# Kernel optimization log

Hardware: AMD Instinct MI355X
Metric: run time of the kernel (lower is better)

The kernel has to match this reference:

```python
import jax, jax.numpy as jnp
import numpy as np

D = 768
H = 16
DH = D // H  # 48
SCALE = 1.0 / np.sqrt(DH).astype(np.float32)
EPS = 1e-3  # keras LayerNormalization default epsilon
NEG = -1e9


def setup_inputs() -> dict:
    key = jax.random.key(0)
    ks = jax.random.split(key, 10)
    B, S = 4, 2048
    q = jax.random.normal(ks[0], (B, S, D), dtype=jnp.float32)
    k = jax.random.normal(ks[1], (B, S, D), dtype=jnp.float32)
    v = jax.random.normal(ks[2], (B, S, D), dtype=jnp.float32)
    # Dense projection params (glorot-ish scale)
    w_std = 1.0 / np.sqrt(D)
    Wq = jax.random.normal(ks[3], (D, D), dtype=jnp.float32) * w_std
    Wk = jax.random.normal(ks[4], (D, D), dtype=jnp.float32) * w_std
    Wv = jax.random.normal(ks[5], (D, D), dtype=jnp.float32) * w_std
    bq = jnp.zeros((D,), jnp.float32)
    bk = jnp.zeros((D,), jnp.float32)
    bv = jnp.zeros((D,), jnp.float32)
    gamma = jnp.ones((D,), jnp.float32)
    beta = jnp.zeros((D,), jnp.float32)
    return {"q": q, "k": k, "v": v, "Wq": Wq, "bq": bq, "Wk": Wk, "bk": bk,
            "Wv": Wv, "bv": bv, "gamma": gamma, "beta": beta}


def reference(q, k, v, Wq, bq, Wk, bk, Wv, bv, gamma, beta):
    use_causal = True  # exercise the causal-mask path
    B, S, _ = q.shape
    # Projections, then split into heads (tf.split on last axis == reshape)
    Q = (q @ Wq + bq).reshape(B, S, H, DH)
    K = (k @ Wk + bk).reshape(B, S, H, DH)
    V = (v @ Wv + bv).reshape(B, S, H, DH)
    # scores: [B, H, Sq, Sk]
    scores = jnp.einsum('bqhd,bkhd->bhqk', Q, K) * SCALE
    if use_causal:
        qi = jnp.arange(S)[:, None]
        ki = jnp.arange(S)[None, :]
        mask = jnp.where(qi >= ki, 0.0, NEG).astype(scores.dtype)
        scores = scores + mask
    attn = jax.nn.softmax(scores, axis=-1)
    out = jnp.einsum('bhqk,bkhd->bqhd', attn, V).reshape(B, S, D)
    # LayerNorm over last dim
    mu = jnp.mean(out, axis=-1, keepdims=True)
    var = jnp.mean(jnp.square(out - mu), axis=-1, keepdims=True)
    return (out - mu) * jax.lax.rsqrt(var + EPS) * gamma + beta
```

## Files before the change

### kernel.cpp

```cpp
#include <hip/hip_runtime.h>
#include <hip/hip_bf16.h>


#define DMODEL 768
#define NHEAD  16
#define DHEAD  48
#define SEQ    2048
#define NBATCH 4
#define NROWS  (NBATCH * SEQ)
#define QSCALE (0.14433756729740643f * 1.4426950408889634f)

typedef __bf16 bf16x8 __attribute__((ext_vector_type(8)));
typedef float  f32x4  __attribute__((ext_vector_type(4)));

__global__ __launch_bounds__(256) void transpose_w(
    const float* __restrict__ Wq,
    const float* __restrict__ Wk,
    const float* __restrict__ Wv,
    __hip_bfloat16* __restrict__ Wt)
{
    __shared__ __hip_bfloat16 tile[32][33];
    int bid = blockIdx.x;
    int mat = bid / 576;
    int t   = bid - mat * 576;
    int tr  = t / 24, tc = t - (t / 24) * 24;
    const float* W = (mat == 0) ? Wq : (mat == 1) ? Wk : Wv;
    __hip_bfloat16* O = Wt + (size_t)mat * DMODEL * DMODEL;
    int tx = threadIdx.x & 31, ty = threadIdx.x >> 5;
#pragma unroll
    for (int i = 0; i < 32; i += 8)
        tile[ty + i][tx] = __float2bfloat16(W[(size_t)(tr * 32 + ty + i) * DMODEL + tc * 32 + tx]);
    __syncthreads();
#pragma unroll
    for (int i = 0; i < 32; i += 8)
        O[(size_t)(tc * 32 + ty + i) * DMODEL + tr * 32 + tx] = tile[tx][ty + i];
}

__global__ __launch_bounds__(256, 2) void qkv_proj(
    const float* __restrict__ xq,
    const float* __restrict__ xk,
    const float* __restrict__ xv,
    const __hip_bfloat16* __restrict__ Wt,
    const float* __restrict__ bq,
    const float* __restrict__ bk,
    const float* __restrict__ bv,
    __hip_bfloat16* __restrict__ Qr,
    __hip_bfloat16* __restrict__ Kr,
    __hip_bfloat16* __restrict__ Vt)
{
    __shared__ __hip_bfloat16 As[2][128 * 32];
    __shared__ __hip_bfloat16 Bs[2][128 * 32];

    int xcd  = blockIdx.x & 7;
    int s    = blockIdx.x >> 3;
    int nt   = s % 6;
    int pair = (s / 6) * 8 + xcd;
    int mat  = pair >> 6;
    int mt   = pair & 63;
    int m0   = mt * 128, n0 = nt * 128;

    const float* X          = (mat == 0) ? xq : (mat == 1) ? xk : xv;
    const __hip_bfloat16* W = Wt + (size_t)mat * DMODEL * DMODEL;
    const float* bias       = (mat == 0) ? bq : (mat == 1) ? bk : bv;

    int tid  = threadIdx.x;
    int w    = tid >> 6, lane = tid & 63;
    int l16  = lane & 15, quad = lane >> 4;
    int wm   = w >> 1, wn = w & 1;

    int rS = tid >> 1;
    int cS = (tid & 1) << 4;
    const float*          xb = X + (size_t)(m0 + rS) * DMODEL + cS;
    const __hip_bfloat16* wb = W + (size_t)(n0 + rS) * DMODEL + cS;
    int ldsOff = rS * 32 + cS;

    float4 fA0, fA1, fA2, fA3;
    uint4  rB0, rB1;

#define QKV_LOAD(k0_) {                                                        \
        fA0 = *(const float4*)(xb + (k0_));                                    \
        fA1 = *(const float4*)(xb + (k0_) + 4);                                \
        fA2 = *(const float4*)(xb + (k0_) + 8);                                \
        fA3 = *(const float4*)(xb + (k0_) + 12);                               \
        rB0 = *(const uint4*)(wb + (k0_));                                     \
        rB1 = *(const uint4*)(wb + (k0_) + 8); }

#define QKV_STORE(buf_) {                                                      \
        *(bf16x8*)&As[buf_][ldsOff] =                                          \
            (bf16x8){ (__bf16)fA0.x, (__bf16)fA0.y, (__bf16)fA0.z, (__bf16)fA0.w, \
                      (__bf16)fA1.x, (__bf16)fA1.y, (__bf16)fA1.z, (__bf16)fA1.w }; \
        *(bf16x8*)&As[buf_][ldsOff + 8] =                                      \
            (bf16x8){ (__bf16)fA2.x, (__bf16)fA2.y, (__bf16)fA2.z, (__bf16)fA2.w, \
                      (__bf16)fA3.x, (__bf16)fA3.y, (__bf16)fA3.z, (__bf16)fA3.w }; \
        *(uint4*)&Bs[buf_][ldsOff]     = rB0;                                  \
        *(uint4*)&Bs[buf_][ldsOff + 8] = rB1; }

    f32x4 acc[4][4] = {};

    QKV_LOAD(0);
    QKV_STORE(0);
    QKV_LOAD(32);
    __syncthreads();

    for (int it = 0; it < 24; ++it) {
        int buf = it & 1;
        if (it + 1 < 24) QKV_STORE(buf ^ 1);
        if (it + 2 < 24) QKV_LOAD((it + 2) * 32);

        bf16x8 a[4], b[4];
#pragma unroll
        for (int i = 0; i < 4; ++i)
            a[i] = *(const bf16x8*)&As[buf][(wm * 64 + i * 16 + l16) * 32 + quad * 8];
#pragma unroll
        for (int j = 0; j < 4; ++j)
            b[j] = *(const bf16x8*)&Bs[buf][(wn * 64 + j * 16 + l16) * 32 + quad * 8];
#pragma unroll
        for (int i = 0; i < 4; ++i)
#pragma unroll
            for (int j = 0; j < 4; ++j)
                acc[i][j] = __builtin_amdgcn_mfma_f32_16x16x32_bf16(a[i], b[j], acc[i][j], 0, 0, 0);

        __syncthreads();
    }
#undef QKV_LOAD
#undef QKV_STORE

#pragma unroll
    for (int j = 0; j < 4; ++j) {
        int col = n0 + wn * 64 + j * 16 + l16;
        float bc = bias[col];
        if (mat == 0) {
#pragma unroll
            for (int i = 0; i < 4; ++i) {
                int row0 = m0 + wm * 64 + i * 16 + quad * 4;
#pragma unroll
                for (int r = 0; r < 4; ++r)
                    Qr[(size_t)(row0 + r) * DMODEL + col] =
                        __float2bfloat16((acc[i][j][r] + bc) * QSCALE);
            }
        } else if (mat == 1) {
#pragma unroll
            for (int i = 0; i < 4; ++i) {
                int row0 = m0 + wm * 64 + i * 16 + quad * 4;
#pragma unroll
                for (int r = 0; r < 4; ++r)
                    Kr[(size_t)(row0 + r) * DMODEL + col] =
                        __float2bfloat16(acc[i][j][r] + bc);
            }
        } else {
            int h = col / 48, dh = col - h * 48;
#pragma unroll
            for (int i = 0; i < 4; ++i) {
                int row0 = m0 + wm * 64 + i * 16 + quad * 4;
                int bb = row0 >> 11, s0 = row0 & 2047;
                ushort4 pk;
                union { __hip_bfloat16 b; unsigned short u; } cv;
                cv.b = __float2bfloat16(acc[i][j][0] + bc); pk.x = cv.u;
                cv.b = __float2bfloat16(acc[i][j][1] + bc); pk.y = cv.u;
                cv.b = __float2bfloat16(acc[i][j][2] + bc); pk.z = cv.u;
                cv.b = __float2bfloat16(acc[i][j][3] + bc); pk.w = cv.u;
                *(ushort4*)(Vt + ((size_t)(bb * NHEAD + h) * DHEAD + dh) * SEQ + s0) = pk;
            }
        }
    }
}

__global__ __launch_bounds__(256, 3) void attn(
    const __hip_bfloat16* __restrict__ Qr,
    const __hip_bfloat16* __restrict__ Kr,
    const __hip_bfloat16* __restrict__ Vt,
    __hip_bfloat16* __restrict__ Ao)
{
    __shared__ __hip_bfloat16 Ks[2][64][72];
    __shared__ __hip_bfloat16 Vs[2][48][72];
    __shared__ __hip_bfloat16 Ps[4][32][72];

    int tid  = threadIdx.x;
    int w    = tid >> 6, lane = tid & 63;
    int l16  = lane & 15, quad = lane >> 4;
    int bh   = blockIdx.x & 63;
    int qt   = 15 - (blockIdx.x >> 6);
    int q0   = qt * 128;
    int b    = bh >> 4, h = bh & 15;
    size_t rowbase = (size_t)b * SEQ;

    const __hip_bfloat16* Qp = Qr + rowbase * DMODEL + h * DHEAD;
    const __hip_bfloat16* Kp = Kr + rowbase * DMODEL + h * DHEAD;
    const __hip_bfloat16* Vp = Vt + (size_t)bh * DHEAD * SEQ;

    for (int idx = tid; idx < 1024; idx += 256) {
        int buf = idx >> 9, r = (idx >> 3) & 63, c = idx & 7;
        ((unsigned int*)&Ks[buf][r][48])[c] = 0u;
    }

    bf16x8 bQ0[2], bQ1[2];
#pragma unroll
    for (int i = 0; i < 2; ++i) {
        int qrow = q0 + w * 32 + i * 16 + l16;
        bQ0[i] = *(const bf16x8*)(Qp + (size_t)qrow * DMODEL + quad * 8);
        bQ1[i] = (bf16x8){};
        if (quad < 2)
            bQ1[i] = *(const bf16x8*)(Qp + (size_t)qrow * DMODEL + 32 + quad * 8);
    }

    int rK = tid >> 2, oK = (tid & 3) * 12;
    int dV = tid >> 3, oV = (tid & 7) * 8;

    uint2 kr0, kr1, kr2; uint4 vr0, vr1;

#define ATTN_LOAD(kt_) {                                                        \
        int k0_ = (kt_) * 64;                                                   \
        const __hip_bfloat16* kb_ = Kp + (size_t)(k0_ + rK) * DMODEL + oK;      \
        kr0 = *(const uint2*)(kb_);                                             \
        kr1 = *(const uint2*)(kb_ + 4);                                         \
        kr2 = *(const uint2*)(kb_ + 8);                                         \
        vr0 = *(const uint4*)(Vp + (size_t)dV * SEQ + k0_ + oV);                \
        if (tid < 128) vr1 = *(const uint4*)(Vp + (size_t)(32 + dV) * SEQ + k0_ + oV); }

#define ATTN_STORE(buf_) {                                                      \
        __hip_bfloat16* kd_ = &Ks[buf_][rK][oK];                                \
        *(uint2*)(kd_)     = kr0;                                               \
        *(uint2*)(kd_ + 4) = kr1;                                               \
        *(uint2*)(kd_ + 8) = kr2;                                               \
        *(uint4*)&Vs[buf_][dV][oV] = vr0;                                       \
        if (tid < 128) *(uint4*)&Vs[buf_][32 + dV][oV] = vr1; }

    f32x4 O[2][3] = {};
    float lsum[2] = {0.f, 0.f};

    int ktmax = 2 * qt + 1;
    ATTN_LOAD(0);
    ATTN_STORE(0);
    if (ktmax >= 1) ATTN_LOAD(1);
    __syncthreads();

    for (int kt = 0; kt <= ktmax; ++kt) {
        int buf = kt & 1;
        int k0  = kt * 64;
        if (kt + 1 <= ktmax) ATTN_STORE(buf ^ 1);
        if (kt + 2 <= ktmax) ATTN_LOAD(kt + 2);

        bf16x8 aK0[4], aK1[4];
#pragma unroll
        for (int t = 0; t < 4; ++t) {
            aK0[t] = *(const bf16x8*)&Ks[buf][16 * t + l16][quad * 8];
            aK1[t] = *(const bf16x8*)&Ks[buf][16 * t + l16][32 + quad * 8];
        }

#pragma unroll
        for (int i = 0; i < 2; ++i) {
            int qbase = q0 + w * 32 + i * 16;
            if (k0 > qbase + 15) continue;

            f32x4 s[4];
#pragma unroll
            for (int t = 0; t < 4; ++t) {
                f32x4 z = {};
                z    = __builtin_amdgcn_mfma_f32_16x16x32_bf16(aK0[t], bQ0[i], z, 0, 0, 0);
                s[t] = __builtin_amdgcn_mfma_f32_16x16x32_bf16(aK1[t], bQ1[i], z, 0, 0, 0);
            }

            if (k0 + 63 > qbase) {
                int qg = qbase + l16;
#pragma unroll
                for (int t = 0; t < 4; ++t) {
                    int kg = k0 + 16 * t + quad * 4;
#pragma unroll
                    for (int r = 0; r < 4; ++r)
                        if (kg + r > qg) s[t][r] = -1e30f;
                }
            }

            float ls = 0.f;
#pragma unroll
            for (int t = 0; t < 4; ++t) {
                float p0 = exp2f(s[t][0]), p1 = exp2f(s[t][1]);
                float p2 = exp2f(s[t][2]), p3 = exp2f(s[t][3]);
                ls += (p0 + p1) + (p2 + p3);
                union { __bf16 hv[4]; uint2 u2; } pk;
                pk.hv[0] = (__bf16)p0; pk.hv[1] = (__bf16)p1;
                pk.hv[2] = (__bf16)p2; pk.hv[3] = (__bf16)p3;
                *(uint2*)&Ps[w][i * 16 + l16][16 * t + quad * 4] = pk.u2;
            }
            lsum[i] += ls;
        }

        bf16x8 bV0[3], bV1[3];
#pragma unroll
        for (int dt = 0; dt < 3; ++dt) {
            bV0[dt] = *(const bf16x8*)&Vs[buf][dt * 16 + l16][quad * 8];
            bV1[dt] = *(const bf16x8*)&Vs[buf][dt * 16 + l16][32 + quad * 8];
        }

#pragma unroll
        for (int i = 0; i < 2; ++i) {
            int qbase = q0 + w * 32 + i * 16;
            if (k0 > qbase + 15) continue;
            bf16x8 aP0 = *(const bf16x8*)&Ps[w][i * 16 + l16][quad * 8];
            bf16x8 aP1 = *(const bf16x8*)&Ps[w][i * 16 + l16][32 + quad * 8];
#pragma unroll
            for (int dt = 0; dt < 3; ++dt) {
                O[i][dt] = __builtin_amdgcn_mfma_f32_16x16x32_bf16(aP0, bV0[dt], O[i][dt], 0, 0, 0);
                O[i][dt] = __builtin_amdgcn_mfma_f32_16x16x32_bf16(aP1, bV1[dt], O[i][dt], 0, 0, 0);
            }
        }

        __syncthreads();
    }

#pragma unroll
    for (int i = 0; i < 2; ++i) {
        lsum[i] += __shfl_xor(lsum[i], 16, 64);
        lsum[i] += __shfl_xor(lsum[i], 32, 64);
    }

#pragma unroll
    for (int i = 0; i < 2; ++i) {
#pragma unroll
        for (int r = 0; r < 4; ++r) {
            float linv = 1.f / __shfl(lsum[i], quad * 4 + r, 64);
            size_t g = (rowbase + q0 + w * 32 + i * 16 + quad * 4 + r) * DMODEL + h * DHEAD + l16;
            Ao[g + 0]  = __float2bfloat16(O[i][0][r] * linv);
            Ao[g + 16] = __float2bfloat16(O[i][1][r] * linv);
            Ao[g + 32] = __float2bfloat16(O[i][2][r] * linv);
        }
    }
#undef ATTN_LOAD
#undef ATTN_STORE
}

__global__ __launch_bounds__(192) void lnorm(
    const __hip_bfloat16* __restrict__ Ao,
    const float* __restrict__ gamma,
    const float* __restrict__ beta,
    float* __restrict__ out)
{
    __shared__ float rs_[3], rq_[3];
    int row = blockIdx.x;
    int t   = threadIdx.x;
    size_t base = (size_t)row * DMODEL + t * 4;

    ushort4 u = *(const ushort4*)(Ao + base);
    float x0, x1, x2, x3;
    { unsigned int v = (unsigned int)u.x << 16; __builtin_memcpy(&x0, &v, 4); }
    { unsigned int v = (unsigned int)u.y << 16; __builtin_memcpy(&x1, &v, 4); }
    { unsigned int v = (unsigned int)u.z << 16; __builtin_memcpy(&x2, &v, 4); }
    { unsigned int v = (unsigned int)u.w << 16; __builtin_memcpy(&x3, &v, 4); }

    float s = x0 + x1 + x2 + x3;
    float q = x0 * x0 + x1 * x1 + x2 * x2 + x3 * x3;
#pragma unroll
    for (int m = 32; m >= 1; m >>= 1) {
        s += __shfl_xor(s, m, 64);
        q += __shfl_xor(q, m, 64);
    }
    int wv = t >> 6;
    if ((t & 63) == 0) { rs_[wv] = s; rq_[wv] = q; }
    __syncthreads();
    float ts = rs_[0] + rs_[1] + rs_[2];
    float tq = rq_[0] + rq_[1] + rq_[2];
    float mu  = ts * (1.f / 768.f);
    float var = tq * (1.f / 768.f) - mu * mu;
    float rstd = rsqrtf(var + 1e-3f);

    float4 g  = *(const float4*)(gamma + t * 4);
    float4 be = *(const float4*)(beta + t * 4);
    float4 o;
    o.x = (x0 - mu) * rstd * g.x + be.x;
    o.y = (x1 - mu) * rstd * g.y + be.y;
    o.z = (x2 - mu) * rstd * g.z + be.z;
    o.w = (x3 - mu) * rstd * g.w + be.w;
    *(float4*)(out + base) = o;
}

extern "C" void kernel_launch(void* const* d_in, const int* in_sizes, int n_in,
                              void* d_out, int out_size, void* d_ws, size_t ws_size,
                              hipStream_t stream) {
    const float* q     = (const float*)d_in[0];
    const float* k     = (const float*)d_in[1];
    const float* v     = (const float*)d_in[2];
    const float* Wq    = (const float*)d_in[3];
    const float* bq    = (const float*)d_in[4];
    const float* Wk    = (const float*)d_in[5];
    const float* bk    = (const float*)d_in[6];
    const float* Wv    = (const float*)d_in[7];
    const float* bv    = (const float*)d_in[8];
    const float* gamma = (const float*)d_in[9];
    const float* beta  = (const float*)d_in[10];

    char* basep = (char*)d_ws;
    __hip_bfloat16* Wt = (__hip_bfloat16*)basep;
    __hip_bfloat16* Qr = (__hip_bfloat16*)(basep + 3538944);
    __hip_bfloat16* Kr = Qr + (size_t)NROWS * DMODEL;
    __hip_bfloat16* Vt = Kr + (size_t)NROWS * DMODEL;
    __hip_bfloat16* Ao = Vt + (size_t)NROWS * DMODEL;
    float* out = (float*)d_out;

    hipLaunchKernelGGL(transpose_w, dim3(1728), dim3(256), 0, stream, Wq, Wk, Wv, Wt);
    hipLaunchKernelGGL(qkv_proj, dim3(1152), dim3(256), 0, stream,
                       q, k, v, Wt, bq, bk, bv, Qr, Kr, Vt);
    hipLaunchKernelGGL(attn, dim3(1024), dim3(256), 0, stream, Qr, Kr, Vt, Ao);
    hipLaunchKernelGGL(lnorm, dim3(8192), dim3(192), 0, stream, Ao, gamma, beta, out);
}
```

Measured before the change: 265.6 us.

## Swizzle QKV GEMM LDS layout, double-register prefetch, and use lighter barriers

The QKV projection GEMM now stages tiles with an XOR-swizzled LDS layout, so the MFMA fragment reads avoid bank conflicts. The loop is unrolled by two with two register sets (A/B), so global loads for tile k+2 are in flight while tile k is computed. __syncthreads is replaced by an explicit lgkmcnt wait plus s_barrier, here and in the attention loop, so outstanding global loads (vmcnt) are not drained at each barrier. This raises register pressure and depends on the manual wait being enough for correctness.

```diff
diff --git a/kernel.cpp b/kernel.cpp
--- a/kernel.cpp
+++ b/kernel.cpp
@@ -67,63 +67,82 @@
     int w    = tid >> 6, lane = tid & 63;
     int l16  = lane & 15, quad = lane >> 4;
     int wm   = w >> 1, wn = w & 1;
-
-    int rS = tid >> 1;
-    int cS = (tid & 1) << 4;
-    const float*          xb = X + (size_t)(m0 + rS) * DMODEL + cS;
-    const __hip_bfloat16* wb = W + (size_t)(n0 + rS) * DMODEL + cS;
-    int ldsOff = rS * 32 + cS;
-
-    float4 fA0, fA1, fA2, fA3;
-    uint4  rB0, rB1;
-
-#define QKV_LOAD(k0_) {                                                        \
-        fA0 = *(const float4*)(xb + (k0_));                                    \
-        fA1 = *(const float4*)(xb + (k0_) + 4);                                \
-        fA2 = *(const float4*)(xb + (k0_) + 8);                                \
-        fA3 = *(const float4*)(xb + (k0_) + 12);                               \
-        rB0 = *(const uint4*)(wb + (k0_));                                     \
-        rB1 = *(const uint4*)(wb + (k0_) + 8); }
-
-#define QKV_STORE(buf_) {                                                      \
-        *(bf16x8*)&As[buf_][ldsOff] =                                          \
-            (bf16x8){ (__bf16)fA0.x, (__bf16)fA0.y, (__bf16)fA0.z, (__bf16)fA0.w, \
-                      (__bf16)fA1.x, (__bf16)fA1.y, (__bf16)fA1.z, (__bf16)fA1.w }; \
-        *(bf16x8*)&As[buf_][ldsOff + 8] =                                      \
-            (bf16x8){ (__bf16)fA2.x, (__bf16)fA2.y, (__bf16)fA2.z, (__bf16)fA2.w, \
-                      (__bf16)fA3.x, (__bf16)fA3.y, (__bf16)fA3.z, (__bf16)fA3.w }; \
-        *(uint4*)&Bs[buf_][ldsOff]     = rB0;                                  \
-        *(uint4*)&Bs[buf_][ldsOff + 8] = rB1; }
+    int qs   = quad ^ ((l16 >> 1) & 3);
+
+    int w0 = tid, w1 = tid + 256;
+    int r0 = w0 >> 2, k0c = (w0 & 3) ^ ((w0 >> 3) & 3);
+    int r1 = w1 >> 2, k1c = (w1 & 3) ^ ((w1 >> 3) & 3);
+    const float*          xb0 = X + (size_t)(m0 + r0) * DMODEL + k0c * 8;
+    const float*          xb1 = X + (size_t)(m0 + r1) * DMODEL + k1c * 8;
+    const __hip_bfloat16* wb0 = W + (size_t)(n0 + r0) * DMODEL + k0c * 8;
+    const __hip_bfloat16* wb1 = W + (size_t)(n0 + r1) * DMODEL + k1c * 8;
+
+    float4 fA0A, fA1A, fA2A, fA3A; uint4 rB0A, rB1A;
+    float4 fA0B, fA1B, fA2B, fA3B; uint4 rB0B, rB1B;
+
+#define QKV_LOAD(kt_, S) {                                                     \
+        fA0##S = *(const float4*)(xb0 + (kt_) * 32);                           \
+        fA1##S = *(const float4*)(xb0 + (kt_) * 32 + 4);                       \
+        fA2##S = *(const float4*)(xb1 + (kt_) * 32);                           \
+        fA3##S = *(const float4*)(xb1 + (kt_) * 32 + 4);                       \
+        rB0##S = *(const uint4*)(wb0 + (kt_) * 32);                            \
+        rB1##S = *(const uint4*)(wb1 + (kt_) * 32); }
+
+#define QKV_STORE(buf_, S) {                                                   \
+        *(bf16x8*)&As[buf_][w0 * 8] =                                          \
+            (bf16x8){ (__bf16)fA0##S.x, (__bf16)fA0##S.y, (__bf16)fA0##S.z, (__bf16)fA0##S.w, \
+                      (__bf16)fA1##S.x, (__bf16)fA1##S.y, (__bf16)fA1##S.z, (__bf16)fA1##S.w }; \
+        *(bf16x8*)&As[buf_][w1 * 8] =                                          \
+            (bf16x8){ (__bf16)fA2##S.x, (__bf16)fA2##S.y, (__bf16)fA2##S.z, (__bf16)fA2##S.w, \
+                      (__bf16)fA3##S.x, (__bf16)fA3##S.y, (__bf16)fA3##S.z, (__bf16)fA3##S.w }; \
+        *(uint4*)&Bs[buf_][w0 * 8] = rB0##S;                                   \
+        *(uint4*)&Bs[buf_][w1 * 8] = rB1##S; }
+
+#define QKV_MATH(buf_) {                                                       \
+        bf16x8 a[4], b[4];                                                     \
+        _Pragma("unroll")                                                      \
+        for (int i = 0; i < 4; ++i)                                            \
+            a[i] = *(const bf16x8*)&As[buf_][(wm * 64 + i * 16 + l16) * 32 + qs * 8]; \
+        _Pragma("unroll")                                                      \
+        for (int j = 0; j < 4; ++j)                                            \
+            b[j] = *(const bf16x8*)&Bs[buf_][(wn * 64 + j * 16 + l16) * 32 + qs * 8]; \
+        _Pragma("unroll")                                                      \
+        for (int i = 0; i < 4; ++i)                                            \
+        _Pragma("unroll")                                                      \
+        for (int j = 0; j < 4; ++j)                                            \
+            acc[i][j] = __builtin_amdgcn_mfma_f32_16x16x32_bf16(a[i], b[j], acc[i][j], 0, 0, 0); }
+
+#define QKV_BARRIER() {                                                        \
+        asm volatile("s_waitcnt lgkmcnt(0)" ::: "memory");                     \
+        __builtin_amdgcn_s_barrier();                                          \
+        asm volatile("" ::: "memory"); }
 
     f32x4 acc[4][4] = {};
 
-    QKV_LOAD(0);
-    QKV_STORE(0);
-    QKV_LOAD(32);
-    __syncthreads();
-
-    for (int it = 0; it < 24; ++it) {
-        int buf = it & 1;
-        if (it + 1 < 24) QKV_STORE(buf ^ 1);
-        if (it + 2 < 24) QKV_LOAD((it + 2) * 32);
-
-        bf16x8 a[4], b[4];
-#pragma unroll
-        for (int i = 0; i < 4; ++i)
-            a[i] = *(const bf16x8*)&As[buf][(wm * 64 + i * 16 + l16) * 32 + quad * 8];
-#pragma unroll
-        for (int j = 0; j < 4; ++j)
-            b[j] = *(const bf16x8*)&Bs[buf][(wn * 64 + j * 16 + l16) * 32 + quad * 8];
-#pragma unroll
-        for (int i = 0; i < 4; ++i)
-#pragma unroll
-            for (int j = 0; j < 4; ++j)
-                acc[i][j] = __builtin_amdgcn_mfma_f32_16x16x32_bf16(a[i], b[j], acc[i][j], 0, 0, 0);
-
-        __syncthreads();
-    }
+    QKV_LOAD(0, A);
+    QKV_STORE(0, A);
+    QKV_LOAD(1, B);
+    QKV_BARRIER();
+
+    for (int it = 0; it < 22; it += 2) {
+        QKV_LOAD(it + 2, A);
+        QKV_STORE(1, B);
+        QKV_MATH(0);
+        QKV_BARRIER();
+        QKV_LOAD(it + 3, B);
+        QKV_STORE(0, A);
+        QKV_MATH(1);
+        QKV_BARRIER();
+    }
+    QKV_STORE(1, B);
+    QKV_MATH(0);
+    QKV_BARRIER();
+    QKV_MATH(1);
+
 #undef QKV_LOAD
 #undef QKV_STORE
+#undef QKV_MATH
+#undef QKV_BARRIER
 
 #pragma unroll
     for (int j = 0; j < 4; ++j) {
@@ -305,7 +324,9 @@
             }
         }
 
-        __syncthreads();
+        asm volatile("s_waitcnt lgkmcnt(0)" ::: "memory");
+        __builtin_amdgcn_s_barrier();
+        asm volatile("" ::: "memory");
     }
 
 #pragma unroll
```

After: 264.4 us. About the same (-0.5%).

## Pre-convert inputs to bf16 and pipeline QKV GEMM with direct global-to-LDS loads

Applied to the files above, without the earlier changes.

A prep kernel now converts the activations to bf16 in scratch space (reusing the output and attention buffers) alongside the weight transpose. The QKV projection is restructured into 512-thread 256x128 tiles that use global_load_lds with a triple-buffered A and double-buffered B, split MFMA phases with priority boosts and explicit waitcnt/barriers. This removes the fp32 register staging and in-loop conversion, and moves more of the loads off the register path. In exchange it adds an extra bf16 write and read of the activations. The attention loop barrier is also replaced with an explicit lgkmcnt wait plus s_barrier.

```diff
diff --git a/kernel.cpp b/kernel.cpp
--- a/kernel.cpp
+++ b/kernel.cpp
@@ -13,33 +13,56 @@
 typedef __bf16 bf16x8 __attribute__((ext_vector_type(8)));
 typedef float  f32x4  __attribute__((ext_vector_type(4)));
 
-__global__ __launch_bounds__(256) void transpose_w(
+__global__ __launch_bounds__(256) void prep(
     const float* __restrict__ Wq,
     const float* __restrict__ Wk,
     const float* __restrict__ Wv,
-    __hip_bfloat16* __restrict__ Wt)
-{
-    __shared__ __hip_bfloat16 tile[32][33];
-    int bid = blockIdx.x;
-    int mat = bid / 576;
-    int t   = bid - mat * 576;
-    int tr  = t / 24, tc = t - (t / 24) * 24;
-    const float* W = (mat == 0) ? Wq : (mat == 1) ? Wk : Wv;
-    __hip_bfloat16* O = Wt + (size_t)mat * DMODEL * DMODEL;
-    int tx = threadIdx.x & 31, ty = threadIdx.x >> 5;
-#pragma unroll
-    for (int i = 0; i < 32; i += 8)
-        tile[ty + i][tx] = __float2bfloat16(W[(size_t)(tr * 32 + ty + i) * DMODEL + tc * 32 + tx]);
-    __syncthreads();
-#pragma unroll
-    for (int i = 0; i < 32; i += 8)
-        O[(size_t)(tc * 32 + ty + i) * DMODEL + tr * 32 + tx] = tile[tx][ty + i];
-}
-
-__global__ __launch_bounds__(256, 2) void qkv_proj(
     const float* __restrict__ xq,
     const float* __restrict__ xk,
     const float* __restrict__ xv,
+    __hip_bfloat16* __restrict__ Wt,
+    __hip_bfloat16* __restrict__ Xbq,
+    __hip_bfloat16* __restrict__ Xbk,
+    __hip_bfloat16* __restrict__ Xbv)
+{
+    int bid = blockIdx.x;
+    if (bid < 1728) {
+        __shared__ __hip_bfloat16 tile[32][33];
+        int mat = bid / 576;
+        int t   = bid - mat * 576;
+        int tr  = t / 24, tc = t - (t / 24) * 24;
+        const float* W = (mat == 0) ? Wq : (mat == 1) ? Wk : Wv;
+        __hip_bfloat16* O = Wt + (size_t)mat * DMODEL * DMODEL;
+        int tx = threadIdx.x & 31, ty = threadIdx.x >> 5;
+#pragma unroll
+        for (int i = 0; i < 32; i += 8)
+            tile[ty + i][tx] = __float2bfloat16(W[(size_t)(tr * 32 + ty + i) * DMODEL + tc * 32 + tx]);
+        __syncthreads();
+#pragma unroll
+        for (int i = 0; i < 32; i += 8)
+            O[(size_t)(tc * 32 + ty + i) * DMODEL + tr * 32 + tx] = tile[tx][ty + i];
+    } else {
+        int b2  = bid - 1728;
+        int mat = b2 / 3072;
+        int r   = b2 - mat * 3072;
+        const float* X = (mat == 0) ? xq : (mat == 1) ? xk : xv;
+        __hip_bfloat16* O = (mat == 0) ? Xbq : (mat == 1) ? Xbk : Xbv;
+        size_t off = (size_t)r * 2048 + threadIdx.x * 8;
+        float4 f0 = *(const float4*)(X + off);
+        float4 f1 = *(const float4*)(X + off + 4);
+        union { __hip_bfloat16 h[8]; uint4 u; } pk;
+        pk.h[0] = __float2bfloat16(f0.x); pk.h[1] = __float2bfloat16(f0.y);
+        pk.h[2] = __float2bfloat16(f0.z); pk.h[3] = __float2bfloat16(f0.w);
+        pk.h[4] = __float2bfloat16(f1.x); pk.h[5] = __float2bfloat16(f1.y);
+        pk.h[6] = __float2bfloat16(f1.z); pk.h[7] = __float2bfloat16(f1.w);
+        *(uint4*)(O + off) = pk.u;
+    }
+}
+
+__global__ __launch_bounds__(512, 4) void qkv_proj(
+    const __hip_bfloat16* __restrict__ Xbq,
+    const __hip_bfloat16* __restrict__ Xbk,
+    const __hip_bfloat16* __restrict__ Xbv,
     const __hip_bfloat16* __restrict__ Wt,
     const float* __restrict__ bq,
     const float* __restrict__ bk,
@@ -48,82 +71,100 @@
     __hip_bfloat16* __restrict__ Kr,
     __hip_bfloat16* __restrict__ Vt)
 {
-    __shared__ __hip_bfloat16 As[2][128 * 32];
-    __shared__ __hip_bfloat16 Bs[2][128 * 32];
-
-    int xcd  = blockIdx.x & 7;
-    int s    = blockIdx.x >> 3;
-    int nt   = s % 6;
-    int pair = (s / 6) * 8 + xcd;
-    int mat  = pair >> 6;
-    int mt   = pair & 63;
-    int m0   = mt * 128, n0 = nt * 128;
-
-    const float* X          = (mat == 0) ? xq : (mat == 1) ? xk : xv;
-    const __hip_bfloat16* W = Wt + (size_t)mat * DMODEL * DMODEL;
-    const float* bias       = (mat == 0) ? bq : (mat == 1) ? bk : bv;
+    __shared__ __hip_bfloat16 Abuf[3][8192];
+    __shared__ __hip_bfloat16 Bbuf[2][4096];
 
     int tid  = threadIdx.x;
     int w    = tid >> 6, lane = tid & 63;
     int l16  = lane & 15, quad = lane >> 4;
     int wm   = w >> 1, wn = w & 1;
 
-    int rS = tid >> 1;
-    int cS = (tid & 1) << 4;
-    const float*          xb = X + (size_t)(m0 + rS) * DMODEL + cS;
-    const __hip_bfloat16* wb = W + (size_t)(n0 + rS) * DMODEL + cS;
-    int ldsOff = rS * 32 + cS;
-
-    float4 fA0, fA1, fA2, fA3;
-    uint4  rB0, rB1;
-
-#define QKV_LOAD(k0_) {                                                        \
-        fA0 = *(const float4*)(xb + (k0_));                                    \
-        fA1 = *(const float4*)(xb + (k0_) + 4);                                \
-        fA2 = *(const float4*)(xb + (k0_) + 8);                                \
-        fA3 = *(const float4*)(xb + (k0_) + 12);                               \
-        rB0 = *(const uint4*)(wb + (k0_));                                     \
-        rB1 = *(const uint4*)(wb + (k0_) + 8); }
-
-#define QKV_STORE(buf_) {                                                      \
-        *(bf16x8*)&As[buf_][ldsOff] =                                          \
-            (bf16x8){ (__bf16)fA0.x, (__bf16)fA0.y, (__bf16)fA0.z, (__bf16)fA0.w, \
-                      (__bf16)fA1.x, (__bf16)fA1.y, (__bf16)fA1.z, (__bf16)fA1.w }; \
-        *(bf16x8*)&As[buf_][ldsOff + 8] =                                      \
-            (bf16x8){ (__bf16)fA2.x, (__bf16)fA2.y, (__bf16)fA2.z, (__bf16)fA2.w, \
-                      (__bf16)fA3.x, (__bf16)fA3.y, (__bf16)fA3.z, (__bf16)fA3.w }; \
-        *(uint4*)&Bs[buf_][ldsOff]     = rB0;                                  \
-        *(uint4*)&Bs[buf_][ldsOff + 8] = rB1; }
+    int xcd = blockIdx.x & 7, s = blockIdx.x >> 3;
+    int nt  = s % 6;
+    int idx = (s / 6) * 8 + xcd;
+    int mat = idx >> 5, mt = idx & 31;
+    int m0  = mt * 256, n0 = nt * 128;
+
+    const __hip_bfloat16* X = (mat == 0) ? Xbq : (mat == 1) ? Xbk : Xbv;
+    const __hip_bfloat16* W = Wt + (size_t)mat * DMODEL * DMODEL;
+    const float* bias       = (mat == 0) ? bq : (mat == 1) ? bk : bv;
+
+    int sr = tid >> 2, sc = (tid & 3) * 8;
+    const __hip_bfloat16* ga0 = X + (size_t)(m0 + sr) * DMODEL + sc;
+    const __hip_bfloat16* ga1 = X + (size_t)(m0 + 128 + sr) * DMODEL + sc;
+    const __hip_bfloat16* gb  = W + (size_t)(n0 + sr) * DMODEL + sc;
+
+#define GLD(gp_, lp_) __builtin_amdgcn_global_load_lds(                        \
+        (const __attribute__((address_space(1))) void*)(gp_),                  \
+        (__attribute__((address_space(3))) void*)(lp_), 16, 0, 0)
+
+    int aoff = (wm * 64 + l16) * 32 + quad * 8;
+    int boff = (wn * 64 + l16) * 32 + quad * 8;
 
     f32x4 acc[4][4] = {};
 
-    QKV_LOAD(0);
-    QKV_STORE(0);
-    QKV_LOAD(32);
-    __syncthreads();
-
-    for (int it = 0; it < 24; ++it) {
-        int buf = it & 1;
-        if (it + 1 < 24) QKV_STORE(buf ^ 1);
-        if (it + 2 < 24) QKV_LOAD((it + 2) * 32);
-
-        bf16x8 a[4], b[4];
-#pragma unroll
-        for (int i = 0; i < 4; ++i)
-            a[i] = *(const bf16x8*)&As[buf][(wm * 64 + i * 16 + l16) * 32 + quad * 8];
-#pragma unroll
-        for (int j = 0; j < 4; ++j)
-            b[j] = *(const bf16x8*)&Bs[buf][(wn * 64 + j * 16 + l16) * 32 + quad * 8];
-#pragma unroll
-        for (int i = 0; i < 4; ++i)
-#pragma unroll
-            for (int j = 0; j < 4; ++j)
-                acc[i][j] = __builtin_amdgcn_mfma_f32_16x16x32_bf16(a[i], b[j], acc[i][j], 0, 0, 0);
-
-        __syncthreads();
-    }
-#undef QKV_LOAD
-#undef QKV_STORE
+    GLD(gb,       &Bbuf[0][tid * 8]);
+    GLD(ga0,      &Abuf[0][tid * 8]);
+    GLD(ga1,      &Abuf[0][4096 + tid * 8]);
+    GLD(ga0 + 32, &Abuf[1][tid * 8]);
+    GLD(ga1 + 32, &Abuf[1][4096 + tid * 8]);
+    asm volatile("s_waitcnt vmcnt(2)" ::: "memory");
+    asm volatile("s_barrier" ::: "memory");
+
+    int abuf = 0, bbuf = 0, abS = 2;
+    const __hip_bfloat16* gbS  = gb  + 32;
+    const __hip_bfloat16* ga0S = ga0 + 64;
+    const __hip_bfloat16* ga1S = ga1 + 64;
+
+    for (int kt = 0; kt < 24; ++kt) {
+        const __hip_bfloat16* LA = Abuf[abuf];
+        const __hip_bfloat16* LB = Bbuf[bbuf];
+
+        bf16x8 a[4], bA[2];
+#pragma unroll
+        for (int m_ = 0; m_ < 4; ++m_)
+            a[m_] = *(const bf16x8*)&LA[aoff + m_ * 512];
+        bA[0] = *(const bf16x8*)&LB[boff];
+        bA[1] = *(const bf16x8*)&LB[boff + 512];
+
+        if (kt < 23) { GLD(gbS, &Bbuf[bbuf ^ 1][tid * 8]); gbS += 32; }
+        if (kt < 22) {
+            GLD(ga0S, &Abuf[abS][tid * 8]);
+            GLD(ga1S, &Abuf[abS][4096 + tid * 8]);
+            ga0S += 32; ga1S += 32;
+        }
+
+        asm volatile("s_barrier" ::: "memory");
+        __builtin_amdgcn_s_setprio(1);
+#pragma unroll
+        for (int m_ = 0; m_ < 4; ++m_) {
+            acc[m_][0] = __builtin_amdgcn_mfma_f32_16x16x32_bf16(a[m_], bA[0], acc[m_][0], 0, 0, 0);
+            acc[m_][1] = __builtin_amdgcn_mfma_f32_16x16x32_bf16(a[m_], bA[1], acc[m_][1], 0, 0, 0);
+        }
+        __builtin_amdgcn_s_setprio(0);
+        asm volatile("s_barrier" ::: "memory");
+
+        bf16x8 bB[2];
+        bB[0] = *(const bf16x8*)&LB[boff + 1024];
+        bB[1] = *(const bf16x8*)&LB[boff + 1536];
+
+        if (kt < 22) asm volatile("s_waitcnt vmcnt(2)" ::: "memory");
+        else         asm volatile("s_waitcnt vmcnt(0)" ::: "memory");
+        asm volatile("s_barrier" ::: "memory");
+        __builtin_amdgcn_s_setprio(1);
+#pragma unroll
+        for (int m_ = 0; m_ < 4; ++m_) {
+            acc[m_][2] = __builtin_amdgcn_mfma_f32_16x16x32_bf16(a[m_], bB[0], acc[m_][2], 0, 0, 0);
+            acc[m_][3] = __builtin_amdgcn_mfma_f32_16x16x32_bf16(a[m_], bB[1], acc[m_][3], 0, 0, 0);
+        }
+        __builtin_amdgcn_s_setprio(0);
+        asm volatile("s_barrier" ::: "memory");
+
+        abuf = (abuf == 2) ? 0 : abuf + 1;
+        abS  = (abS  == 2) ? 0 : abS  + 1;
+        bbuf ^= 1;
+    }
+#undef GLD
 
 #pragma unroll
     for (int j = 0; j < 4; ++j) {
@@ -305,7 +346,9 @@
             }
         }
 
-        __syncthreads();
+        asm volatile("s_waitcnt lgkmcnt(0)" ::: "memory");
+        __builtin_amdgcn_s_barrier();
+        asm volatile("" ::: "memory");
     }
 
 #pragma unroll
@@ -396,9 +439,14 @@
     __hip_bfloat16* Ao = Vt + (size_t)NROWS * DMODEL;
     float* out = (float*)d_out;
 
-    hipLaunchKernelGGL(transpose_w, dim3(1728), dim3(256), 0, stream, Wq, Wk, Wv, Wt);
-    hipLaunchKernelGGL(qkv_proj, dim3(1152), dim3(256), 0, stream,
-                       q, k, v, Wt, bq, bk, bv, Qr, Kr, Vt);
+    __hip_bfloat16* Xbq = (__hip_bfloat16*)d_out;
+    __hip_bfloat16* Xbk = Xbq + (size_t)NROWS * DMODEL;
+    __hip_bfloat16* Xbv = Ao;
+
+    hipLaunchKernelGGL(prep, dim3(10944), dim3(256), 0, stream,
+                       Wq, Wk, Wv, q, k, v, Wt, Xbq, Xbk, Xbv);
+    hipLaunchKernelGGL(qkv_proj, dim3(576), dim3(512), 0, stream,
+                       Xbq, Xbk, Xbv, Wt, bq, bk, bv, Qr, Kr, Vt);
     hipLaunchKernelGGL(attn, dim3(1024), dim3(256), 0, stream, Qr, Kr, Vt, Ao);
     hipLaunchKernelGGL(lnorm, dim3(8192), dim3(192), 0, stream, Ao, gamma, beta, out);
 }
```

Result: faster. 256.3 us (-3.5%).
